# Kernel tuning notes

Hardware: AMD Instinct MI355X
Metric: run time of the kernel (lower is better)

Reference implementation:

```python
import jax, jax.numpy as jnp
import numpy as np

E = 128          # embed_dim
CTX = 3 * E      # context_dim = 384 (graph_emb 2E + node_emb E)
B = 16
N = 1024
D_IN = 2 * CTX   # mamba inner dim (expand=2) = 768
D_ST = 16        # mamba_hidden_dim (SSM state size)
DT_R = CTX // 16 # dt_rank = 24
K = 4            # causal depthwise conv kernel
TAU = 1.0        # gs_tau
ITERS = 5        # gs_iters


def setup_inputs() -> dict:
    key = jax.random.key(0)
    ks = jax.random.split(key, 12)
    s = 0.02
    inp = {
        "graph_emb": jax.random.normal(ks[0], (B, 2 * E), jnp.float32),
        "node_emb": jax.random.normal(ks[1], (B, N, E), jnp.float32),
        "W_key": jax.random.normal(ks[2], (E, CTX), jnp.float32) * s,
        "rms_w": jnp.ones((CTX,), jnp.float32),
        "W_in": jax.random.normal(ks[3], (CTX, 2 * D_IN), jnp.float32) * s,
        "conv_w": jax.random.normal(ks[4], (D_IN, K), jnp.float32) * s,
        "conv_b": jnp.zeros((D_IN,), jnp.float32),
        "W_x": jax.random.normal(ks[5], (D_IN, DT_R + 2 * D_ST), jnp.float32) * s,
        "W_dt": jax.random.normal(ks[6], (DT_R, D_IN), jnp.float32) * s,
        "b_dt": jnp.full((D_IN,), -4.0, jnp.float32),  # softplus -> small positive dt
        "A_log": jnp.log(jnp.tile(jnp.arange(1, D_ST + 1, dtype=jnp.float32), (D_IN, 1))),
        "Dp": jnp.ones((D_IN,), jnp.float32),
        "W_out": jax.random.normal(ks[7], (D_IN, CTX), jnp.float32) * s,
        "gumbel_sink": jax.random.gumbel(ks[8], (B, N, N), jnp.float32),
        "gumbel_sample": jax.random.gumbel(ks[9], (B, N, N), jnp.float32),
    }
    return inp


def _mamba(x, rms_w, W_in, conv_w, conv_b, W_x, W_dt, b_dt, A_log, Dp, W_out):
    # x: (B, N, CTX) -> (B, N, CTX); RMSNorm -> S6 mixer -> residual
    h = x * jax.lax.rsqrt(jnp.mean(x * x, axis=-1, keepdims=True) + 1e-6) * rms_w
    u, z = jnp.split(h @ W_in, 2, axis=-1)              # each (B, N, D_IN)
    # causal depthwise conv over the sequence axis
    uc = jnp.transpose(u, (0, 2, 1))                    # (B, D_IN, N)
    uc = jax.lax.conv_general_dilated(
        uc, conv_w[:, None, :], (1,), [(K - 1, 0)],
        dimension_numbers=("NCH", "OIH", "NCH"), feature_group_count=D_IN)
    u = jax.nn.silu(jnp.transpose(uc, (0, 2, 1)) + conv_b)  # (B, N, D_IN)
    dbc = u @ W_x                                       # (B, N, DT_R + 2*D_ST)
    dt, Bm, Cm = jnp.split(dbc, [DT_R, DT_R + D_ST], axis=-1)
    delta = jax.nn.softplus(dt @ W_dt + b_dt)           # (B, N, D_IN)
    A = -jnp.exp(A_log)                                 # (D_IN, D_ST)

    def step(hst, t):
        u_t, d_t, B_t, C_t = t                          # (B,D_IN),(B,D_IN),(B,D_ST),(B,D_ST)
        dA = jnp.exp(d_t[:, :, None] * A)               # (B, D_IN, D_ST)
        hst = dA * hst + (d_t * u_t)[:, :, None] * B_t[:, None, :]
        y = jnp.sum(hst * C_t[:, None, :], axis=-1)     # (B, D_IN)
        return hst, y

    seq = (jnp.transpose(u, (1, 0, 2)), jnp.transpose(delta, (1, 0, 2)),
           jnp.transpose(Bm, (1, 0, 2)), jnp.transpose(Cm, (1, 0, 2)))
    h0 = jnp.zeros((x.shape[0], D_IN, D_ST), x.dtype)
    _, ys = jax.lax.scan(step, h0, seq)                 # ys: (N, B, D_IN)
    y = jnp.transpose(ys, (1, 0, 2)) + Dp * u
    y = y * jax.nn.silu(z)
    return x + y @ W_out


def reference(graph_emb, node_emb, W_key, rms_w, W_in, conv_w, conv_b, W_x,
              W_dt, b_dt, A_log, Dp, W_out, gumbel_sink, gumbel_sample):
    b, n, _ = node_emb.shape
    keys = node_emb @ W_key                             # (B, N, CTX)
    ctx = jnp.concatenate(
        [jnp.broadcast_to(graph_emb[:, None, :], (b, n, graph_emb.shape[-1])), node_emb], axis=-1)
    queries = _mamba(ctx, rms_w, W_in, conv_w, conv_b, W_x, W_dt, b_dt, A_log, Dp, W_out)
    logits = jnp.einsum("bic,bjc->bij", keys, queries)  # (B, N, N)
    # Gumbel-Sinkhorn in log domain; end on row (axis=2) normalization -> rows are log-probs
    la = (logits + gumbel_sink) / TAU
    for _ in range(ITERS):
        la = la - jax.nn.logsumexp(la, axis=1, keepdims=True)  # column scaling
        la = la - jax.nn.logsumexp(la, axis=2, keepdims=True)  # row scaling
    # sampled tour: per-step categorical via Gumbel-max over rows
    tours = jnp.argmax(la + gumbel_sample, axis=-1)     # (B, N) int
    log_probs = jnp.take_along_axis(la, tours[..., None], axis=2)[..., 0]  # (B, N)
    entropies = -jnp.sum(la * jnp.exp(la), axis=-1)     # (B, N)
    return tours, log_probs, entropies
```

## Files before the change

kernel.cpp:

```cpp
#include <hip/hip_runtime.h>
#include <math.h>

#define Bsz 16
#define Nn  1024
#define Ee  128
#define CTX 384
#define DIN 768
#define DST 16
#define DTR 24
#define ROWS (Bsz*Nn)

__global__ __launch_bounds__(128) void rms_k(
    const float* __restrict__ ge, const float* __restrict__ ne,
    float* __restrict__ rs)
{
    int row = blockIdx.x;
    int b = row >> 10;
    int tid = threadIdx.x;
    float ssq = 0.f;
    #pragma unroll
    for (int k = 0; k < 3; ++k) {
        int idx = tid + k * 128;
        float v = (idx < 256) ? ge[b * 256 + idx]
                              : ne[(long long)row * 128 + (idx - 256)];
        ssq += v * v;
    }
    __shared__ float sh[128];
    sh[tid] = ssq;
    __syncthreads();
    for (int w = 64; w > 0; w >>= 1) {
        if (tid < w) sh[tid] += sh[tid + w];
        __syncthreads();
    }
    if (tid == 0) rs[row] = rsqrtf(sh[0] * (1.f / 384.f) + 1e-6f);
}

__global__ __launch_bounds__(256) void zero_k(float* __restrict__ p, int n)
{
    int i = blockIdx.x * 256 + threadIdx.x;
    if (i < n) p[i] = 0.f;
}

template<int EPI, bool BT, int AMODE, bool CT>
__global__ __launch_bounds__(256) void gemm2_k(
    const float* __restrict__ A, int lda, long long aB,
    const float* __restrict__ Bm, int ldb, long long bB,
    float* __restrict__ C, int ldc, long long cB,
    int M, int N, int K,
    const float* __restrict__ ge, const float* __restrict__ ne,
    const float* __restrict__ rowS, const float* __restrict__ colS,
    const float* __restrict__ bias,
    const float* __restrict__ add, long long addB)
{
    __shared__ float As[16][132];
    __shared__ float Bs[16][132];
    int t = threadIdx.x;
    int gn0 = blockIdx.x * 128;
    int rowBase = blockIdx.y * 128;
    int bz = blockIdx.z;
    const float* Abase = A + (long long)bz * aB;
    const float* Bb = Bm + (long long)bz * bB;
    float acc[8][8] = {};

    int cx4 = (t & 15) * 4;
    int ry4 = (t >> 4) * 4;

    for (int k0 = 0; k0 < K; k0 += 16) {
        if (AMODE == 0 || AMODE == 1) {
            int r = t >> 1;
            int kq = (t & 1) * 8;
            float av[8];
            if (AMODE == 0) {
                const float* Ap = Abase + (long long)(rowBase + r) * lda + k0 + kq;
                #pragma unroll
                for (int j = 0; j < 8; ++j)
                    av[j] = (k0 + kq + j < K) ? Ap[j] : 0.f;
            } else {
                int grow = rowBase + r;
                float rsv = rowS[grow];
                #pragma unroll
                for (int j = 0; j < 8; ++j) {
                    int col = k0 + kq + j;
                    float v = 0.f;
                    if (col < K) {
                        v = (col < 256) ? ge[(grow >> 10) * 256 + col]
                                        : ne[(long long)grow * 128 + (col - 256)];
                        v *= rsv * colS[col];
                    }
                    av[j] = v;
                }
            }
            #pragma unroll
            for (int j = 0; j < 8; ++j) As[kq + j][r] = av[j];
        } else {
            int kk = t >> 4;
            int m0 = (t & 15) * 8;
            const float* Ap = Abase + (long long)(k0 + kk) * lda + rowBase + m0;
            float4 v0 = make_float4(0.f, 0.f, 0.f, 0.f), v1 = v0;
            if (k0 + kk < K) {
                v0 = *(const float4*)Ap;
                v1 = *(const float4*)(Ap + 4);
            }
            *(float4*)&As[kk][m0] = v0;
            *(float4*)&As[kk][m0 + 4] = v1;
        }
        if (!BT) {
            int kk = t >> 4;
            int n0 = (t & 15) * 8;
            const float* Bp = Bb + (long long)(k0 + kk) * ldb + gn0 + n0;
            float4 v0 = make_float4(0.f, 0.f, 0.f, 0.f), v1 = v0;
            if (k0 + kk < K) {
                if (gn0 + n0 + 7 < N) {
                    v0 = *(const float4*)Bp;
                    v1 = *(const float4*)(Bp + 4);
                } else {
                    float tmp[8];
                    #pragma unroll
                    for (int j = 0; j < 8; ++j)
                        tmp[j] = (gn0 + n0 + j < N) ? Bp[j] : 0.f;
                    v0 = make_float4(tmp[0], tmp[1], tmp[2], tmp[3]);
                    v1 = make_float4(tmp[4], tmp[5], tmp[6], tmp[7]);
                }
            }
            *(float4*)&Bs[kk][n0] = v0;
            *(float4*)&Bs[kk][n0 + 4] = v1;
        } else {
            int n = t >> 1;
            int kq = (t & 1) * 8;
            const float* Bp = Bb + (long long)(gn0 + n) * ldb + k0 + kq;
            float bv[8];
            bool nok = (gn0 + n < N);
            #pragma unroll
            for (int j = 0; j < 8; ++j)
                bv[j] = (nok && k0 + kq + j < K) ? Bp[j] : 0.f;
            #pragma unroll
            for (int j = 0; j < 8; ++j) Bs[kq + j][n] = bv[j];
        }
        __syncthreads();
        #pragma unroll
        for (int kk = 0; kk < 16; ++kk) {
            float4 a0 = *(const float4*)&As[kk][ry4];
            float4 a1 = *(const float4*)&As[kk][ry4 + 64];
            float4 b0 = *(const float4*)&Bs[kk][cx4];
            float4 b1 = *(const float4*)&Bs[kk][cx4 + 64];
            float av[8] = {a0.x, a0.y, a0.z, a0.w, a1.x, a1.y, a1.z, a1.w};
            float bv[8] = {b0.x, b0.y, b0.z, b0.w, b1.x, b1.y, b1.z, b1.w};
            #pragma unroll
            for (int i = 0; i < 8; ++i)
                #pragma unroll
                for (int j = 0; j < 8; ++j)
                    acc[i][j] = fmaf(av[i], bv[j], acc[i][j]);
        }
        __syncthreads();
    }

    if (CT) {
        #pragma unroll
        for (int j = 0; j < 8; ++j) {
            int gn = gn0 + (j >> 2) * 64 + cx4 + (j & 3);
            #pragma unroll
            for (int ih = 0; ih < 2; ++ih) {
                int gmb = rowBase + ih * 64 + ry4;
                float4 v = make_float4(acc[ih * 4 + 0][j], acc[ih * 4 + 1][j],
                                       acc[ih * 4 + 2][j], acc[ih * 4 + 3][j]);
                *(float4*)&C[(long long)gn * ldc + gmb] = v;
            }
        }
    } else {
        float* Cb = C + (long long)bz * cB;
        #pragma unroll
        for (int i = 0; i < 8; ++i) {
            int gm = rowBase + (i >> 2) * 64 + ry4 + (i & 3);
            #pragma unroll
            for (int jh = 0; jh < 2; ++jh) {
                int gn = gn0 + jh * 64 + cx4;
                float v[4];
                #pragma unroll
                for (int e = 0; e < 4; ++e) {
                    float x = acc[i][jh * 4 + e];
                    if (EPI == 3) {
                        x += add[(long long)bz * addB + (long long)gm * (long long)N + gn + e];
                    } else if (EPI == 4) {
                        int c = gn + e;
                        x += (c < 256) ? ge[(gm >> 10) * 256 + c]
                                       : ne[(long long)gm * 128 + (c - 256)];
                    } else if (EPI == 5) {
                        float s = x + bias[gm];
                        x = fmaxf(s, 0.f) + log1pf(expf(-fabsf(s)));
                    }
                    v[e] = x;
                }
                if (gn + 3 < N) {
                    *(float4*)&Cb[(long long)gm * ldc + gn] =
                        make_float4(v[0], v[1], v[2], v[3]);
                } else {
                    #pragma unroll
                    for (int e = 0; e < 4; ++e)
                        if (gn + e < N) Cb[(long long)gm * ldc + gn + e] = v[e];
                }
            }
        }
    }
}

__global__ __launch_bounds__(256) void conv_t_k(
    const float* __restrict__ uB, const float* __restrict__ cw,
    const float* __restrict__ cb, float* __restrict__ uT)
{
    __shared__ float tile[67][33];
    int b = blockIdx.z, d0 = blockIdx.y * 32, n0 = blockIdx.x * 64;
    int tid = threadIdx.x;
    for (int i = tid; i < 67 * 32; i += 256) {
        int r = i >> 5, c = i & 31;
        int n = n0 - 3 + r;
        tile[r][c] = (n >= 0) ? uB[((long long)(b * 1024 + n)) * 768 + d0 + c] : 0.f;
    }
    __syncthreads();
    int nl = tid & 63;
    int dh = (tid >> 6) * 8;
    #pragma unroll
    for (int dl = 0; dl < 8; ++dl) {
        int d = dh + dl;
        const float* w = cw + (d0 + d) * 4;
        float acc = cb[d0 + d];
        acc = fmaf(tile[nl][d],     w[0], acc);
        acc = fmaf(tile[nl + 1][d], w[1], acc);
        acc = fmaf(tile[nl + 2][d], w[2], acc);
        acc = fmaf(tile[nl + 3][d], w[3], acc);
        float sv = acc / (1.f + __expf(-acc));
        uT[(long long)(d0 + d) * 16384 + b * 1024 + n0 + nl] = sv;
    }
}

__global__ __launch_bounds__(256) void pack_bc_k(
    const float* __restrict__ dbc, float* __restrict__ TBC)
{
    int c = blockIdx.y;
    int gm = blockIdx.x * 256 + threadIdx.x;
    TBC[(long long)c * 16384 + gm] = dbc[(long long)gm * 56 + 24 + c];
}

__global__ __launch_bounds__(256) void scan3_k(
    const float* __restrict__ dT, float* uyT, const float* __restrict__ zT,
    const float* __restrict__ TBC, const float* __restrict__ A_log,
    const float* __restrict__ Dp)
{
    int tid = threadIdx.x;
    int s = tid & 15, dl = tid >> 4;
    int b = blockIdx.y;
    int d = blockIdx.x * 16 + dl;
    float a = -__expf(A_log[d * 16 + s]);
    float dp = Dp[d];
    long long base = (long long)b * 1024;
    const float* dR = dT + (long long)d * 16384 + base;
    const float* uR = uyT + (long long)d * 16384 + base;
    const float* zR = zT + (long long)d * 16384 + base;
    const float* BR = TBC + (long long)s * 16384 + base;
    const float* CR = TBC + (long long)(16 + s) * 16384 + base;
    float* yR = uyT + (long long)d * 16384 + base;

    float4 dv0 = *(const float4*)(dR);
    float4 dv1 = *(const float4*)(dR + 4);
    float4 uv0 = *(const float4*)(uR);
    float4 uv1 = *(const float4*)(uR + 4);
    float4 zv0 = *(const float4*)(zR);
    float4 zv1 = *(const float4*)(zR + 4);
    float4 Bv0 = *(const float4*)(BR);
    float4 Bv1 = *(const float4*)(BR + 4);
    float4 Cv0 = *(const float4*)(CR);
    float4 Cv1 = *(const float4*)(CR + 4);
    float h = 0.f;

    for (int g = 0; g < 256; ++g) {
        int gp = (g + 2 < 256) ? (g + 2) * 4 : 255 * 4;
        float4 dv2 = *(const float4*)(dR + gp);
        float4 uv2 = *(const float4*)(uR + gp);
        float4 zv2 = *(const float4*)(zR + gp);
        float4 Bv2 = *(const float4*)(BR + gp);
        float4 Cv2 = *(const float4*)(CR + gp);

        float dv[4] = {dv0.x, dv0.y, dv0.z, dv0.w};
        float uv[4] = {uv0.x, uv0.y, uv0.z, uv0.w};
        float zv[4] = {zv0.x, zv0.y, zv0.z, zv0.w};
        float Bv[4] = {Bv0.x, Bv0.y, Bv0.z, Bv0.w};
        float Cv[4] = {Cv0.x, Cv0.y, Cv0.z, Cv0.w};
        float ya[4];
        #pragma unroll
        for (int j = 0; j < 4; ++j) {
            float dA = __expf(dv[j] * a);
            h = fmaf(dA, h, dv[j] * uv[j] * Bv[j]);
            float yp = h * Cv[j];
            yp += __shfl_down(yp, 8, 16);
            yp += __shfl_down(yp, 4, 16);
            yp += __shfl_down(yp, 2, 16);
            yp += __shfl_down(yp, 1, 16);
            float z = zv[j];
            ya[j] = (yp + dp * uv[j]) * (z / (1.f + __expf(-z)));
        }
        if (s == 0) {
            *(float4*)(yR + g * 4) = make_float4(ya[0], ya[1], ya[2], ya[3]);
        }
        dv0 = dv1; dv1 = dv2;
        uv0 = uv1; uv1 = uv2;
        zv0 = zv1; zv1 = zv2;
        Bv0 = Bv1; Bv1 = Bv2;
        Cv0 = Cv1; Cv1 = Cv2;
    }
}

__global__ __launch_bounds__(256) void col_lse_part(
    const float* __restrict__ la0, const float* __restrict__ R,
    float2* __restrict__ cpart)
{
    int j = blockIdx.x * 256 + threadIdx.x;
    int ch = blockIdx.y;
    int b = blockIdx.z;
    const float* base = la0 + (long long)b * 1024 * 1024 + (long long)ch * 64 * 1024 + j;
    const float* Rb = R + b * 1024 + ch * 64;
    float m = -INFINITY, sum = 0.f;
    for (int i = 0; i < 64; ++i) {
        float x = base[(long long)i * 1024] - Rb[i];
        float nm = fmaxf(m, x);
        sum = sum * expf(m - nm) + expf(x - nm);
        m = nm;
    }
    cpart[(long long)(b * 16 + ch) * 1024 + j] = make_float2(m, sum);
}

__global__ __launch_bounds__(256) void col_comb_k(
    const float2* __restrict__ cpart, float* __restrict__ Cv)
{
    int idx = blockIdx.x * 256 + threadIdx.x;
    int b = idx >> 10, j = idx & 1023;
    float m = -INFINITY, sum = 0.f;
    #pragma unroll
    for (int ch = 0; ch < 16; ++ch) {
        float2 p = cpart[(long long)(b * 16 + ch) * 1024 + j];
        float nm = fmaxf(m, p.x);
        sum = sum * expf(m - nm) + p.y * expf(p.x - nm);
        m = nm;
    }
    Cv[idx] = m + logf(sum);
}

__global__ __launch_bounds__(256) void row_lse_k(
    const float* __restrict__ la0, const float* __restrict__ Cv,
    float* __restrict__ R)
{
    int r = blockIdx.x;
    int b = r >> 10;
    const float* row = la0 + (long long)r * 1024;
    const float* Cb = Cv + b * 1024;
    int tid = threadIdx.x;
    float m = -INFINITY, sum = 0.f;
    #pragma unroll
    for (int k = 0; k < 4; ++k) {
        int j = tid + k * 256;
        float x = row[j] - Cb[j];
        float nm = fmaxf(m, x);
        sum = sum * expf(m - nm) + expf(x - nm);
        m = nm;
    }
    __shared__ float sm[256], ss[256];
    sm[tid] = m; ss[tid] = sum;
    __syncthreads();
    for (int w = 128; w > 0; w >>= 1) {
        if (tid < w) {
            float m2 = sm[tid + w], s2 = ss[tid + w];
            float nm = fmaxf(sm[tid], m2);
            ss[tid] = ss[tid] * expf(sm[tid] - nm) + s2 * expf(m2 - nm);
            sm[tid] = nm;
        }
        __syncthreads();
    }
    if (tid == 0) R[r] = sm[0] + logf(ss[0]);
}

__global__ __launch_bounds__(256) void final_k(
    const float* __restrict__ la0, const float* __restrict__ R,
    const float* __restrict__ Cv, const float* __restrict__ gs,
    float* __restrict__ out)
{
    int r = blockIdx.x;
    int b = r >> 10;
    const float* row = la0 + (long long)r * 1024;
    const float* gr = gs + (long long)r * 1024;
    const float* Cb = Cv + b * 1024;
    float Rvv = R[r];
    int tid = threadIdx.x;
    float bestg = -INFINITY;
    int bestj = 1 << 30;
    float ent = 0.f;
    #pragma unroll
    for (int k = 0; k < 4; ++k) {
        int j = tid + k * 256;
        float la = row[j] - Rvv - Cb[j];
        ent += la * expf(la);
        float g = la + gr[j];
        if (g > bestg || (g == bestg && j < bestj)) { bestg = g; bestj = j; }
    }
    __shared__ float sg[256]; __shared__ int sj[256]; __shared__ float se[256];
    sg[tid] = bestg; sj[tid] = bestj; se[tid] = ent;
    __syncthreads();
    for (int w = 128; w > 0; w >>= 1) {
        if (tid < w) {
            se[tid] += se[tid + w];
            float g2 = sg[tid + w]; int j2 = sj[tid + w];
            if (g2 > sg[tid] || (g2 == sg[tid] && j2 < sj[tid])) {
                sg[tid] = g2; sj[tid] = j2;
            }
        }
        __syncthreads();
    }
    if (tid == 0) {
        int j = sj[0];
        out[r] = (float)j;
        out[16384 + r] = row[j] - Rvv - Cb[j];
        out[32768 + r] = -se[0];
    }
}

extern "C" void kernel_launch(void* const* d_in, const int* in_sizes, int n_in,
                              void* d_out, int out_size, void* d_ws, size_t ws_size,
                              hipStream_t stream)
{
    const float* graph_emb = (const float*)d_in[0];
    const float* node_emb  = (const float*)d_in[1];
    const float* W_key     = (const float*)d_in[2];
    const float* rms_w     = (const float*)d_in[3];
    const float* W_in      = (const float*)d_in[4];
    const float* conv_w    = (const float*)d_in[5];
    const float* conv_b    = (const float*)d_in[6];
    const float* W_x       = (const float*)d_in[7];
    const float* W_dt      = (const float*)d_in[8];
    const float* b_dt      = (const float*)d_in[9];
    const float* A_log     = (const float*)d_in[10];
    const float* Dp        = (const float*)d_in[11];
    const float* W_out     = (const float*)d_in[12];
    const float* g_sink    = (const float*)d_in[13];
    const float* g_samp    = (const float*)d_in[14];
    float* out = (float*)d_out;

    float* ws = (float*)d_ws;
    size_t o = 0;
    auto alloc = [&](size_t nf) { float* p = ws + o; o += nf; return p; };
    float* rs    = alloc(ROWS);
    float* dbc   = alloc((size_t)ROWS * 56);
    float* keys  = alloc((size_t)ROWS * 384);
    float* R1    = alloc((size_t)ROWS * 768);
    float* R2    = alloc((size_t)ROWS * 768);
    float* R3    = alloc((size_t)ROWS * 768);
    float* Rv    = alloc(ROWS);
    float* Cvec  = alloc(ROWS);
    float* cpart = alloc((size_t)16 * 16 * 1024 * 2);
    float* uB      = R1;
    float* deltaT  = R1;
    float* queries = R1;
    float* uT      = R2;
    float* zT      = R3;
    float* la0     = R2;
    float* TBC     = cpart;

    rms_k<<<dim3(ROWS), 128, 0, stream>>>(graph_emb, node_emb, rs);

    gemm2_k<0, false, 0, false><<<dim3(3, 128, 1), 256, 0, stream>>>(
        node_emb, 128, 0, W_key, 384, 0, keys, 384, 0,
        ROWS, 384, 128, nullptr, nullptr, nullptr, nullptr, nullptr, nullptr, 0);

    gemm2_k<0, false, 1, false><<<dim3(6, 128, 1), 256, 0, stream>>>(
        nullptr, 0, 0, W_in, 1536, 0, uB, 768, 0,
        ROWS, 768, 384, graph_emb, node_emb, rs, rms_w, nullptr, nullptr, 0);

    gemm2_k<0, false, 1, true><<<dim3(6, 128, 1), 256, 0, stream>>>(
        nullptr, 0, 0, W_in + 768, 1536, 0, zT, 16384, 0,
        ROWS, 768, 384, graph_emb, node_emb, rs, rms_w, nullptr, nullptr, 0);

    conv_t_k<<<dim3(16, 24, 16), 256, 0, stream>>>(uB, conv_w, conv_b, uT);

    gemm2_k<0, false, 2, false><<<dim3(1, 128, 1), 256, 0, stream>>>(
        uT, 16384, 0, W_x, 56, 0, dbc, 56, 0,
        ROWS, 56, 768, nullptr, nullptr, nullptr, nullptr, nullptr, nullptr, 0);

    gemm2_k<5, true, 2, false><<<dim3(128, 6, 1), 256, 0, stream>>>(
        W_dt, 768, 0, dbc, 56, 0, deltaT, 16384, 0,
        768, 16384, 24, nullptr, nullptr, nullptr, nullptr, b_dt, nullptr, 0);

    pack_bc_k<<<dim3(64, 32), 256, 0, stream>>>(dbc, TBC);

    scan3_k<<<dim3(48, 16), 256, 0, stream>>>(deltaT, uT, zT, TBC, A_log, Dp);

    gemm2_k<4, false, 2, false><<<dim3(3, 128, 1), 256, 0, stream>>>(
        uT, 16384, 0, W_out, 384, 0, queries, 384, 0,
        ROWS, 384, 768, graph_emb, node_emb, nullptr, nullptr, nullptr, nullptr, 0);

    gemm2_k<3, true, 0, false><<<dim3(8, 8, 16), 256, 0, stream>>>(
        keys, 384, (long long)Nn * 384, queries, 384, (long long)Nn * 384,
        la0, 1024, (long long)Nn * Nn,
        1024, 1024, 384, nullptr, nullptr, nullptr, nullptr, nullptr,
        g_sink, (long long)Nn * Nn);

    zero_k<<<dim3(64), 256, 0, stream>>>(Rv, ROWS);
    for (int it = 0; it < 5; ++it) {
        col_lse_part<<<dim3(4, 16, 16), 256, 0, stream>>>(la0, Rv, (float2*)cpart);
        col_comb_k<<<dim3(64), 256, 0, stream>>>((const float2*)cpart, Cvec);
        row_lse_k<<<dim3(ROWS), 256, 0, stream>>>(la0, Cvec, Rv);
    }

    final_k<<<dim3(ROWS), 256, 0, stream>>>(la0, Rv, Cvec, g_samp, out);
}
```

Measured before the change: 1.604 ms.

## Chunk the selective scan along sequence with two-pass carry propagation

Replaces the sequential per-(d,state) scan with a chunked scan. Each thread now handles 4 states over a quarter of the sequence: a first pass computes chunk-local states and decay products, a shared-memory step combines the carries across the 4 chunks, and a second pass recomputes the recurrence from the correct initial state and produces outputs. B and C are read directly from dbc, which removes the separate pack kernel. The goal is to cut the serial dependency length by a factor of four, at the cost of computing the recurrence twice and using strided, uncoalesced reads of B and C.

```diff
diff --git a/kernel.cpp b/kernel.cpp
--- a/kernel.cpp
+++ b/kernel.cpp
@@ -232,79 +232,122 @@
     }
 }
 
-__global__ __launch_bounds__(256) void pack_bc_k(
-    const float* __restrict__ dbc, float* __restrict__ TBC)
-{
-    int c = blockIdx.y;
-    int gm = blockIdx.x * 256 + threadIdx.x;
-    TBC[(long long)c * 16384 + gm] = dbc[(long long)gm * 56 + 24 + c];
-}
-
-__global__ __launch_bounds__(256) void scan3_k(
+__global__ __launch_bounds__(256, 3) void scan4_k(
     const float* __restrict__ dT, float* uyT, const float* __restrict__ zT,
-    const float* __restrict__ TBC, const float* __restrict__ A_log,
+    const float* __restrict__ dbc, const float* __restrict__ A_log,
     const float* __restrict__ Dp)
 {
-    int tid = threadIdx.x;
-    int s = tid & 15, dl = tid >> 4;
+    __shared__ float sH[4][16][16];
+    __shared__ float sP[4][16][16];
+    __shared__ float sh0[4][16][16];
+    int t = threadIdx.x;
+    int ch = t >> 4;
+    int sq = (t >> 2) & 3;
+    int c  = t & 3;
     int b = blockIdx.y;
-    int d = blockIdx.x * 16 + dl;
-    float a = -__expf(A_log[d * 16 + s]);
+    int d = blockIdx.x * 16 + ch;
+    float av[4];
+    #pragma unroll
+    for (int j = 0; j < 4; ++j) av[j] = -__expf(A_log[d * 16 + 4 * sq + j]);
     float dp = Dp[d];
-    long long base = (long long)b * 1024;
-    const float* dR = dT + (long long)d * 16384 + base;
-    const float* uR = uyT + (long long)d * 16384 + base;
-    const float* zR = zT + (long long)d * 16384 + base;
-    const float* BR = TBC + (long long)s * 16384 + base;
-    const float* CR = TBC + (long long)(16 + s) * 16384 + base;
-    float* yR = uyT + (long long)d * 16384 + base;
-
-    float4 dv0 = *(const float4*)(dR);
-    float4 dv1 = *(const float4*)(dR + 4);
-    float4 uv0 = *(const float4*)(uR);
-    float4 uv1 = *(const float4*)(uR + 4);
-    float4 zv0 = *(const float4*)(zR);
-    float4 zv1 = *(const float4*)(zR + 4);
-    float4 Bv0 = *(const float4*)(BR);
-    float4 Bv1 = *(const float4*)(BR + 4);
-    float4 Cv0 = *(const float4*)(CR);
-    float4 Cv1 = *(const float4*)(CR + 4);
-    float h = 0.f;
-
-    for (int g = 0; g < 256; ++g) {
-        int gp = (g + 2 < 256) ? (g + 2) * 4 : 255 * 4;
-        float4 dv2 = *(const float4*)(dR + gp);
-        float4 uv2 = *(const float4*)(uR + gp);
-        float4 zv2 = *(const float4*)(zR + gp);
-        float4 Bv2 = *(const float4*)(BR + gp);
-        float4 Cv2 = *(const float4*)(CR + gp);
-
-        float dv[4] = {dv0.x, dv0.y, dv0.z, dv0.w};
-        float uv[4] = {uv0.x, uv0.y, uv0.z, uv0.w};
-        float zv[4] = {zv0.x, zv0.y, zv0.z, zv0.w};
-        float Bv[4] = {Bv0.x, Bv0.y, Bv0.z, Bv0.w};
-        float Cv[4] = {Cv0.x, Cv0.y, Cv0.z, Cv0.w};
-        float ya[4];
+    long long base = (long long)d * 16384 + b * 1024 + c * 256;
+    const float* dR = dT + base;
+    const float* uR = uyT + base;
+    const float* zR = zT + base;
+    float* yR = uyT + base;
+    const float* bRow = dbc + (long long)(b * 1024 + c * 256) * 56;
+
+    float hs[4] = {0.f, 0.f, 0.f, 0.f};
+    float Ps[4] = {1.f, 1.f, 1.f, 1.f};
+
+    {
+        float4 dv0 = *(const float4*)(dR);
+        float4 dv1 = *(const float4*)(dR + 4);
+        float4 uv0 = *(const float4*)(uR);
+        float4 uv1 = *(const float4*)(uR + 4);
+        for (int g = 0; g < 64; ++g) {
+            int gp = (g + 2 < 64 ? g + 2 : 63) * 4;
+            float4 dv2 = *(const float4*)(dR + gp);
+            float4 uv2 = *(const float4*)(uR + gp);
+            float dvx[4] = {dv0.x, dv0.y, dv0.z, dv0.w};
+            float uvx[4] = {uv0.x, uv0.y, uv0.z, uv0.w};
+            const float* br = bRow + (long long)(g * 4) * 56 + 24 + 4 * sq;
+            #pragma unroll
+            for (int j = 0; j < 4; ++j) {
+                float4 Bv = *(const float4*)(br + j * 56);
+                float du = dvx[j] * uvx[j];
+                float e;
+                e = __expf(dvx[j] * av[0]); hs[0] = fmaf(e, hs[0], du * Bv.x); Ps[0] *= e;
+                e = __expf(dvx[j] * av[1]); hs[1] = fmaf(e, hs[1], du * Bv.y); Ps[1] *= e;
+                e = __expf(dvx[j] * av[2]); hs[2] = fmaf(e, hs[2], du * Bv.z); Ps[2] *= e;
+                e = __expf(dvx[j] * av[3]); hs[3] = fmaf(e, hs[3], du * Bv.w); Ps[3] *= e;
+            }
+            dv0 = dv1; dv1 = dv2; uv0 = uv1; uv1 = uv2;
+        }
+    }
+
+    #pragma unroll
+    for (int j = 0; j < 4; ++j) {
+        sH[c][ch][4 * sq + j] = hs[j];
+        sP[c][ch][4 * sq + j] = Ps[j];
+    }
+    __syncthreads();
+    {
+        int ch2 = t >> 4, s2 = t & 15;
+        float hh = 0.f;
         #pragma unroll
-        for (int j = 0; j < 4; ++j) {
-            float dA = __expf(dv[j] * a);
-            h = fmaf(dA, h, dv[j] * uv[j] * Bv[j]);
-            float yp = h * Cv[j];
-            yp += __shfl_down(yp, 8, 16);
-            yp += __shfl_down(yp, 4, 16);
-            yp += __shfl_down(yp, 2, 16);
-            yp += __shfl_down(yp, 1, 16);
-            float z = zv[j];
-            ya[j] = (yp + dp * uv[j]) * (z / (1.f + __expf(-z)));
-        }
-        if (s == 0) {
-            *(float4*)(yR + g * 4) = make_float4(ya[0], ya[1], ya[2], ya[3]);
-        }
-        dv0 = dv1; dv1 = dv2;
-        uv0 = uv1; uv1 = uv2;
-        zv0 = zv1; zv1 = zv2;
-        Bv0 = Bv1; Bv1 = Bv2;
-        Cv0 = Cv1; Cv1 = Cv2;
+        for (int c2 = 0; c2 < 4; ++c2) {
+            sh0[c2][ch2][s2] = hh;
+            hh = fmaf(sP[c2][ch2][s2], hh, sH[c2][ch2][s2]);
+        }
+    }
+    __syncthreads();
+    #pragma unroll
+    for (int j = 0; j < 4; ++j) hs[j] = sh0[c][ch][4 * sq + j];
+
+    {
+        float4 dv0 = *(const float4*)(dR);
+        float4 dv1 = *(const float4*)(dR + 4);
+        float4 uv0 = *(const float4*)(uR);
+        float4 uv1 = *(const float4*)(uR + 4);
+        float4 zv0 = *(const float4*)(zR);
+        float4 zv1 = *(const float4*)(zR + 4);
+        for (int g = 0; g < 64; ++g) {
+            int gp = (g + 2 < 64 ? g + 2 : 63) * 4;
+            float4 dv2 = *(const float4*)(dR + gp);
+            float4 uv2 = *(const float4*)(uR + gp);
+            float4 zv2 = *(const float4*)(zR + gp);
+            float dvx[4] = {dv0.x, dv0.y, dv0.z, dv0.w};
+            float uvx[4] = {uv0.x, uv0.y, uv0.z, uv0.w};
+            float zvx[4] = {zv0.x, zv0.y, zv0.z, zv0.w};
+            const float* br = bRow + (long long)(g * 4) * 56 + 24 + 4 * sq;
+            float ya[4];
+            #pragma unroll
+            for (int j = 0; j < 4; ++j) {
+                float4 Bv = *(const float4*)(br + j * 56);
+                float4 Cv = *(const float4*)(br + j * 56 + 16);
+                float du = dvx[j] * uvx[j];
+                float e;
+                e = __expf(dvx[j] * av[0]); hs[0] = fmaf(e, hs[0], du * Bv.x);
+                e = __expf(dvx[j] * av[1]); hs[1] = fmaf(e, hs[1], du * Bv.y);
+                e = __expf(dvx[j] * av[2]); hs[2] = fmaf(e, hs[2], du * Bv.z);
+                e = __expf(dvx[j] * av[3]); hs[3] = fmaf(e, hs[3], du * Bv.w);
+                float yp = hs[0] * Cv.x;
+                yp = fmaf(hs[1], Cv.y, yp);
+                yp = fmaf(hs[2], Cv.z, yp);
+                yp = fmaf(hs[3], Cv.w, yp);
+                yp += __shfl_down(yp, 8, 16);
+                yp += __shfl_down(yp, 4, 16);
+                float z = zvx[j];
+                ya[j] = (yp + dp * uvx[j]) * (z / (1.f + __expf(-z)));
+            }
+            if (sq == 0) {
+                *(float4*)(yR + g * 4) = make_float4(ya[0], ya[1], ya[2], ya[3]);
+            }
+            dv0 = dv1; dv1 = dv2;
+            uv0 = uv1; uv1 = uv2;
+            zv0 = zv1; zv1 = zv2;
+        }
     }
 }
 
@@ -459,7 +502,6 @@
     float* uT      = R2;
     float* zT      = R3;
     float* la0     = R2;
-    float* TBC     = cpart;
 
     rms_k<<<dim3(ROWS), 128, 0, stream>>>(graph_emb, node_emb, rs);
 
@@ -485,9 +527,7 @@
         W_dt, 768, 0, dbc, 56, 0, deltaT, 16384, 0,
         768, 16384, 24, nullptr, nullptr, nullptr, nullptr, b_dt, nullptr, 0);
 
-    pack_bc_k<<<dim3(64, 32), 256, 0, stream>>>(dbc, TBC);
-
-    scan3_k<<<dim3(48, 16), 256, 0, stream>>>(deltaT, uT, zT, TBC, A_log, Dp);
+    scan4_k<<<dim3(48, 16), 256, 0, stream>>>(deltaT, uT, zT, dbc, A_log, Dp);
 
     gemm2_k<4, false, 2, false><<<dim3(3, 128, 1), 256, 0, stream>>>(
         uT, 16384, 0, W_out, 384, 0, queries, 384, 0,
```

Result: slower. 1.706 ms (+6.3%).

## Compute logits GEMM on bf16 MFMA with three-way split for fp32 accuracy

Applied to the files above, without the earlier changes.

Replaces the FP32 SIMT batched GEMM for keys·queriesᵀ with an MFMA kernel. Each fp32 value is split into high, mid and low bf16 parts, and six cross-product terms are packed along K so that 16x16x32 bf16 MFMAs recover near-fp32 precision. The gumbel_sink add is fused into the epilogue. It costs extra conversion work and shared memory per K chunk, uses non-coalesced scalar stores, and has no double buffering.

```diff
diff --git a/kernel.cpp b/kernel.cpp
--- a/kernel.cpp
+++ b/kernel.cpp
@@ -9,6 +9,9 @@
 #define DST 16
 #define DTR 24
 #define ROWS (Bsz*Nn)
+
+typedef __attribute__((ext_vector_type(8))) short short8;
+typedef __attribute__((ext_vector_type(4))) float f32x4;
 
 __global__ __launch_bounds__(128) void rms_k(
     const float* __restrict__ ge, const float* __restrict__ ne,
@@ -203,6 +206,102 @@
     }
 }
 
+#define MG_LDK 104
+
+__device__ inline void split3(float v, ushort& h, ushort& m, ushort& l)
+{
+    unsigned u = __float_as_uint(v);
+    h = (ushort)(u >> 16);
+    float vh = __uint_as_float((unsigned)h << 16);
+    float r = v - vh;
+    unsigned ur = __float_as_uint(r);
+    m = (ushort)(ur >> 16);
+    float vm = __uint_as_float((unsigned)m << 16);
+    float r2 = r - vm;
+    unsigned u2 = __float_as_uint(r2);
+    u2 += 0x7fffu + ((u2 >> 16) & 1u);
+    l = (ushort)(u2 >> 16);
+}
+
+__global__ __launch_bounds__(256) void mgemm_logits_k(
+    const float* __restrict__ keys, const float* __restrict__ queries,
+    const float* __restrict__ gsink, float* __restrict__ la0)
+{
+    __shared__ ushort As[128][MG_LDK];
+    __shared__ ushort Bs[128][MG_LDK];
+    int t = threadIdx.x;
+    int n0 = blockIdx.x * 128, m0 = blockIdx.y * 128, bz = blockIdx.z;
+    const float* Ag = keys    + ((long long)(bz * 1024 + m0)) * 384;
+    const float* Bg = queries + ((long long)(bz * 1024 + n0)) * 384;
+    int wave = t >> 6, lane = t & 63;
+    int wm = (wave & 1) * 64, wn = (wave >> 1) * 64;
+    int lm = lane & 15, lq = lane >> 4;
+    f32x4 acc[4][4] = {};
+
+    for (int kc = 0; kc < 384; kc += 16) {
+        {
+            int r = t & 127;
+            bool isA = (t < 128);
+            const float* src = (isA ? Ag : Bg) + (long long)r * 384 + kc;
+            #pragma unroll
+            for (int q = 0; q < 4; ++q) {
+                float4 v = *(const float4*)(src + q * 4);
+                float vv[4] = {v.x, v.y, v.z, v.w};
+                ushort buf[24];
+                #pragma unroll
+                for (int e = 0; e < 4; ++e) {
+                    ushort h, m, l;
+                    split3(vv[e], h, m, l);
+                    if (isA) {
+                        buf[e*6+0] = h; buf[e*6+1] = h; buf[e*6+2] = m;
+                        buf[e*6+3] = h; buf[e*6+4] = m; buf[e*6+5] = l;
+                    } else {
+                        buf[e*6+0] = h; buf[e*6+1] = m; buf[e*6+2] = h;
+                        buf[e*6+3] = l; buf[e*6+4] = m; buf[e*6+5] = h;
+                    }
+                }
+                ushort* dst = (isA ? &As[r][0] : &Bs[r][0]) + q * 24;
+                #pragma unroll
+                for (int w8 = 0; w8 < 3; ++w8)
+                    *(short8*)(dst + w8 * 8) = *(const short8*)&buf[w8 * 8];
+            }
+        }
+        __syncthreads();
+        #pragma unroll
+        for (int dep = 0; dep < 3; ++dep) {
+            short8 af[4], bf[4];
+            #pragma unroll
+            for (int i = 0; i < 4; ++i)
+                af[i] = *(const short8*)&As[wm + i * 16 + lm][dep * 32 + lq * 8];
+            #pragma unroll
+            for (int j = 0; j < 4; ++j)
+                bf[j] = *(const short8*)&Bs[wn + j * 16 + lm][dep * 32 + lq * 8];
+            #pragma unroll
+            for (int i = 0; i < 4; ++i)
+                #pragma unroll
+                for (int j = 0; j < 4; ++j)
+                    acc[i][j] = __builtin_amdgcn_mfma_f32_16x16x32_bf16(
+                        af[i], bf[j], acc[i][j], 0, 0, 0);
+        }
+        __syncthreads();
+    }
+
+    long long obase = (long long)bz * 1024 * 1024;
+    #pragma unroll
+    for (int i = 0; i < 4; ++i) {
+        #pragma unroll
+        for (int rg = 0; rg < 4; ++rg) {
+            int m = m0 + wm + i * 16 + lq * 4 + rg;
+            #pragma unroll
+            for (int j = 0; j < 4; ++j) {
+                int n = n0 + wn + j * 16 + lm;
+                long long off = obase + (long long)m * 1024 + n;
+                la0[off] = acc[i][j][rg] + gsink[off];
+            }
+        }
+    }
+}
+
 __global__ __launch_bounds__(256) void conv_t_k(
     const float* __restrict__ uB, const float* __restrict__ cw,
     const float* __restrict__ cb, float* __restrict__ uT)
@@ -493,11 +592,7 @@
         uT, 16384, 0, W_out, 384, 0, queries, 384, 0,
         ROWS, 384, 768, graph_emb, node_emb, nullptr, nullptr, nullptr, nullptr, 0);
 
-    gemm2_k<3, true, 0, false><<<dim3(8, 8, 16), 256, 0, stream>>>(
-        keys, 384, (long long)Nn * 384, queries, 384, (long long)Nn * 384,
-        la0, 1024, (long long)Nn * Nn,
-        1024, 1024, 384, nullptr, nullptr, nullptr, nullptr, nullptr,
-        g_sink, (long long)Nn * Nn);
+    mgemm_logits_k<<<dim3(8, 8, 16), 256, 0, stream>>>(keys, queries, g_sink, la0);
 
     zero_k<<<dim3(64), 256, 0, stream>>>(Rv, ROWS);
     for (int it = 0; it < 5; ++it) {
```

Measured after the change: 1.506 ms. 6.1% less time.
